# Kernel optimization log

Measured on AMD Instinct MI355X. Metric: run time of the kernel, lower is better.

## Reference

```python
import jax, jax.numpy as jnp
import numpy as np
from jax import lax

EPS = 1e-5


def _conv(x, w, b, stride, pad):
    # x: [B,C,H,W], w: [O,I,kh,kw] (NCHW / OIHW, same as torch Conv2d)
    y = lax.conv_general_dilated(
        x, w, window_strides=stride,
        padding=[(pad[0], pad[0]), (pad[1], pad[1])],
        dimension_numbers=('NCHW', 'OIHW', 'NCHW'))
    return y + b[None, :, None, None]


def _bn(x, gamma, beta, mean, var):
    # BatchNorm2d in eval mode (running statistics)
    inv = gamma / jnp.sqrt(var + EPS)
    return x * inv[None, :, None, None] + (beta - mean * inv)[None, :, None, None]


def _mask_time(x, lens):
    # Vectorized replacement of the per-sample narrow/fill loop:
    # zero every time step >= lens[b] along the last axis.
    t = jnp.arange(x.shape[3])
    keep = (t[None, :] < lens[:, None]).astype(x.dtype)  # [B, W]
    return x * keep[:, None, None, :]


def _new_len(lens, kernel_w, stride_w, pad_w):
    # matches get_new_sequence_lengths for Conv2d with dilation 1
    return (lens + 2 * pad_w - (kernel_w - 1) - 1) // stride_w + 1


def _forward(inputs, seq_lengths,
             w1, b1, g1, be1, m1, v1,
             w2, b2, g2, be2, m2, v2):
    lens = seq_lengths.astype(jnp.int32)
    # layer 1: Conv2d(1,32,(41,11),(2,2),(20,5))
    x = _conv(inputs, w1, b1, (2, 2), (20, 5))
    lens = _new_len(lens, 11, 2, 5)
    x = _mask_time(x, lens)
    # BatchNorm2d(32) -> mask
    x = _mask_time(_bn(x, g1, be1, m1, v1), lens)
    # Hardtanh(0,20) -> mask
    x = _mask_time(jnp.clip(x, 0.0, 20.0), lens)
    # layer 2: Conv2d(32,32,(21,11),(2,1),(10,5))
    x = _conv(x, w2, b2, (2, 1), (10, 5))
    lens = _new_len(lens, 11, 1, 5)
    x = _mask_time(x, lens)
    x = _mask_time(_bn(x, g2, be2, m2, v2), lens)
    x = _mask_time(jnp.clip(x, 0.0, 20.0), lens)
    return x, lens


def setup_inputs() -> dict:
    key = jax.random.key(0)
    ks = jax.random.split(key, 8)
    inputs = jax.random.normal(ks[0], (32, 1, 161, 1024), dtype=jnp.float32)
    seq_lengths = jax.random.randint(ks[1], (32,), 1, 1024, dtype=jnp.int32)
    w1 = jax.random.normal(ks[2], (32, 1, 41, 11), dtype=jnp.float32) * 0.05
    b1 = jax.random.normal(ks[3], (32,), dtype=jnp.float32) * 0.05
    w2 = jax.random.normal(ks[4], (32, 32, 21, 11), dtype=jnp.float32) * 0.02
    b2 = jax.random.normal(ks[5], (32,), dtype=jnp.float32) * 0.05
    g1 = jnp.ones((32,), jnp.float32)
    be1 = jnp.zeros((32,), jnp.float32)
    m1 = jax.random.normal(ks[6], (32,), dtype=jnp.float32) * 0.1
    v1 = jnp.ones((32,), jnp.float32)
    g2 = jnp.ones((32,), jnp.float32)
    be2 = jnp.zeros((32,), jnp.float32)
    m2 = jax.random.normal(ks[7], (32,), dtype=jnp.float32) * 0.1
    v2 = jnp.ones((32,), jnp.float32)
    return {"inputs": inputs, "seq_lengths": seq_lengths,
            "w1": w1, "b1": b1, "g1": g1, "be1": be1, "m1": m1, "v1": v1,
            "w2": w2, "b2": b2, "g2": g2, "be2": be2, "m2": m2, "v2": v2}


def reference(inputs, seq_lengths, w1, b1, g1, be1, m1, v1,
              w2, b2, g2, be2, m2, v2):
    return _forward(inputs, seq_lengths, w1, b1, g1, be1, m1, v1,
                    w2, b2, g2, be2, m2, v2)
```

## Files before the change

### kernel.cpp

```cpp
#include <hip/hip_runtime.h>
#include <math.h>

#define B_    32
#define H_IN  161
#define W_IN  1024
#define C1_   32
#define H1_   81
#define W1_   512
#define C2_   32
#define H2_   41
#define W2_   512

#define OUT_X_SZ ((size_t)B_ * C2_ * H2_ * W2_)

#define WF2_B    0u
#define WF1_B    473088u
#define SCSH_B   515072u
#define LENS1_B  515584u
#define XG_B     515712u

#define WF2_N    236544
#define WF1_N    20992

typedef __bf16 v8bf __attribute__((ext_vector_type(8)));
typedef float v16f __attribute__((ext_vector_type(16)));

static __device__ __forceinline__ unsigned short f2bf(float f) {
    unsigned int u = __float_as_uint(f);
    unsigned int r = (u + 0x7fffu + ((u >> 16) & 1u)) >> 16;
    return (unsigned short)r;
}

__global__ void prep_kernel(const float* __restrict__ w1, const float* __restrict__ b1,
                            const float* __restrict__ g1, const float* __restrict__ be1,
                            const float* __restrict__ m1, const float* __restrict__ v1,
                            const float* __restrict__ w2, const float* __restrict__ b2,
                            const float* __restrict__ g2, const float* __restrict__ be2,
                            const float* __restrict__ m2, const float* __restrict__ v2,
                            const int* __restrict__ lens,
                            unsigned short* __restrict__ wf1, unsigned short* __restrict__ wf2,
                            float* __restrict__ scsh, int* __restrict__ lens1,
                            float* __restrict__ out_lens)
{
    const int i = blockIdx.x * blockDim.x + threadIdx.x;
    const int stride = gridDim.x * blockDim.x;

    for (int idx = i; idx < WF2_N; idx += stride) {
        int j  = idx & 7;
        int l  = (idx >> 3) & 63;
        int f  = idx >> 9;
        int ch = f & 1;
        int kwkh = f >> 1;
        int kw = kwkh % 11;
        int kh = kwkh / 11;
        int oc = l & 31;
        int c  = ch * 16 + ((l >> 5) << 3) + j;
        wf2[idx] = f2bf(w2[((oc * 32 + c) * 21 + kh) * 11 + kw]);
    }
    for (int idx = i; idx < WF1_N; idx += stride) {
        int j  = idx & 7;
        int l  = (idx >> 3) & 63;
        int kh = idx >> 9;
        int k  = ((l >> 5) << 3) + j;
        int oc = l & 31;
        wf1[idx] = (k < 11) ? f2bf(w1[oc * 451 + kh * 11 + k]) : (unsigned short)0;
    }
    if (i < 32) {
        float s1 = g1[i] / sqrtf(v1[i] + 1e-5f);
        scsh[i]      = s1;
        scsh[32 + i] = b1[i] * s1 + be1[i] - m1[i] * s1;
        float s2 = g2[i] / sqrtf(v2[i] + 1e-5f);
        scsh[64 + i] = s2;
        scsh[96 + i] = b2[i] * s2 + be2[i] - m2[i] * s2;
        int l1 = (lens[i] - 1) / 2 + 1;
        if (l1 > W1_) l1 = W1_;
        lens1[i] = l1;
        out_lens[i] = (float)l1;
    }
}

__global__ __launch_bounds__(256) void conv1_mfma(
    const float* __restrict__ x,
    const unsigned short* __restrict__ wf1,
    const float* __restrict__ scsh,
    const int* __restrict__ lens1,
    unsigned short* __restrict__ xg)
{
    const int t    = threadIdx.x;
    const int lane = t & 63;
    const int l31  = lane & 31;
    const int lhi  = lane >> 5;
    const int wv   = t >> 6;
    const int w0   = blockIdx.x * 256;
    const int h    = blockIdx.y;
    const int b    = blockIdx.z;

    __shared__ unsigned int srow[2][264];

    v16f acc0, acc1;
#pragma unroll
    for (int i = 0; i < 16; ++i) { acc0[i] = 0.f; acc1[i] = 0.f; }

    const int r0 = 2 * h - 20;
    const int cb = 2 * w0 - 5;
    const float* xb = x + (size_t)b * (H_IN * W_IN);

    const int dwbase = wv * 64 + l31 + 4 * lhi;

    {
        float a0 = 0.f, a1 = 0.f, c0v = 0.f, c1v = 0.f;
        if (r0 >= 0 && r0 < H_IN) {
            const float* src = xb + (size_t)r0 * W_IN;
            int c0 = cb + 2 * t;
            if ((unsigned)c0 < (unsigned)W_IN)       a0 = src[c0];
            if ((unsigned)(c0 + 1) < (unsigned)W_IN) a1 = src[c0 + 1];
            if (t < 7) {
                int c1 = cb + 2 * (256 + t);
                if ((unsigned)c1 < (unsigned)W_IN)       c0v = src[c1];
                if ((unsigned)(c1 + 1) < (unsigned)W_IN) c1v = src[c1 + 1];
            }
        }
        srow[0][t] = (unsigned int)f2bf(a0) | ((unsigned int)f2bf(a1) << 16);
        if (t < 7)
            srow[0][256 + t] = (unsigned int)f2bf(c0v) | ((unsigned int)f2bf(c1v) << 16);
    }
    __syncthreads();

    for (int kh = 0; kh < 41; ++kh) {
        const int p = kh & 1;
        const int rn = r0 + kh + 1;
        const bool rv = (kh < 40) && (rn >= 0) && (rn < H_IN);

        float a0 = 0.f, a1 = 0.f, c0v = 0.f, c1v = 0.f;
        if (rv) {
            const float* src = xb + (size_t)rn * W_IN;
            int c0 = cb + 2 * t;
            if ((unsigned)c0 < (unsigned)W_IN)       a0 = src[c0];
            if ((unsigned)(c0 + 1) < (unsigned)W_IN) a1 = src[c0 + 1];
            if (t < 7) {
                int c1 = cb + 2 * (256 + t);
                if ((unsigned)c1 < (unsigned)W_IN)       c0v = src[c1];
                if ((unsigned)(c1 + 1) < (unsigned)W_IN) c1v = src[c1 + 1];
            }
        }

        const int r = r0 + kh;
        if (r >= 0 && r < H_IN) {
            uint4 a_u = *((const uint4*)wf1 + kh * 32 + lane);
            v8bf a = __builtin_bit_cast(v8bf, a_u);
            const unsigned int* bp = &srow[p][0];
            {
                int dw = dwbase;
                uint4 bu;
                bu.x = bp[dw]; bu.y = bp[dw + 1]; bu.z = bp[dw + 2]; bu.w = bp[dw + 3];
                v8bf bb = __builtin_bit_cast(v8bf, bu);
                acc0 = __builtin_amdgcn_mfma_f32_32x32x16_bf16(a, bb, acc0, 0, 0, 0);
            }
            {
                int dw = dwbase + 32;
                uint4 bu;
                bu.x = bp[dw]; bu.y = bp[dw + 1]; bu.z = bp[dw + 2]; bu.w = bp[dw + 3];
                v8bf bb = __builtin_bit_cast(v8bf, bu);
                acc1 = __builtin_amdgcn_mfma_f32_32x32x16_bf16(a, bb, acc1, 0, 0, 0);
            }
        }

        if (rv) {
            srow[p ^ 1][t] = (unsigned int)f2bf(a0) | ((unsigned int)f2bf(a1) << 16);
            if (t < 7)
                srow[p ^ 1][256 + t] = (unsigned int)f2bf(c0v) | ((unsigned int)f2bf(c1v) << 16);
        }
        __syncthreads();
    }

    const int l1 = lens1[b];
#pragma unroll
    for (int nt = 0; nt < 2; ++nt) {
        const int w = w0 + wv * 64 + nt * 32 + l31;
        const bool keep = (w < l1);
        unsigned short* dp = xg + (((size_t)b * H1_ + h) * W1_ + w) * 32;
#pragma unroll
        for (int rq = 0; rq < 4; ++rq) {
            unsigned int wd[2];
#pragma unroll
            for (int d = 0; d < 2; ++d) {
                int rg = rq * 4 + d * 2;
                int oc = 8 * rq + 4 * lhi + d * 2;
                float av0 = (nt == 0) ? acc0[rg]     : acc1[rg];
                float av1 = (nt == 0) ? acc0[rg + 1] : acc1[rg + 1];
                float v0 = fminf(fmaxf(fmaf(av0, scsh[oc],     scsh[32 + oc]), 0.f), 20.f);
                float v1 = fminf(fmaxf(fmaf(av1, scsh[oc + 1], scsh[33 + oc]), 0.f), 20.f);
                if (!keep) { v0 = 0.f; v1 = 0.f; }
                wd[d] = (unsigned int)f2bf(v0) | ((unsigned int)f2bf(v1) << 16);
            }
            uint2 u; u.x = wd[0]; u.y = wd[1];
            *(uint2*)(dp + 8 * rq + 4 * lhi) = u;
        }
    }
}

#define ROWB 21280

__global__ __launch_bounds__(256, 3) void conv2_mfma(
    const unsigned short* __restrict__ xg,
    const unsigned short* __restrict__ wf2,
    const float* __restrict__ scsh,
    const int* __restrict__ lens1,
    float* __restrict__ out)
{
    const int t    = threadIdx.x;
    const int lane = t & 63;
    const int l31  = lane & 31;
    const int lhi  = lane >> 5;
    const int wv   = t >> 6;
    const int w0B  = blockIdx.x * 256;
    const int h    = blockIdx.y;
    const int b    = blockIdx.z;

    __shared__ __align__(16) char sbuf[2 * ROWB];

    v16f acc0, acc1;
#pragma unroll
    for (int i = 0; i < 16; ++i) { acc0[i] = 0.f; acc1[i] = 0.f; }

    const int st_lds = (t >> 2) * 80 + (t & 3) * 16;
    const int rd_lds = (wv * 64 + l31) * 80 + lhi * 16;

    const unsigned short* xb = xg + (size_t)b * (H1_ * W1_ * 32);
    const int r0 = 2 * h - 10;

    {
        int r = r0;
        if (r >= 0 && r < H1_) {
            const unsigned short* xrow = xb + (size_t)r * (W1_ * 32);
#pragma unroll
            for (int it = 0; it < 5; ++it) {
                int i = t + it * 256;
                int wp = (i >> 2) + w0B - 5;
                uint4 z; z.x = z.y = z.z = z.w = 0u;
                if (i < 1064 && wp >= 0 && wp < W1_)
                    z = *(const uint4*)(xrow + (size_t)wp * 32 + (i & 3) * 8);
                if (i < 1064)
                    *(uint4*)(sbuf + st_lds + it * 5120) = z;
            }
        }
    }
    __syncthreads();

    for (int kh = 0; kh < 21; ++kh) {
        const int p = kh & 1;
        const int rn = r0 + kh + 1;
        const bool stage_next = (kh < 20) && (rn >= 0) && (rn < H1_);

        uint4 g0, g1, g2, g3, g4;
        g0.x=g0.y=g0.z=g0.w=0u; g1=g0; g2=g0; g3=g0; g4=g0;
        if (stage_next) {
            const unsigned short* xrow = xb + (size_t)rn * (W1_ * 32);
            const int wbase = (t >> 2) + w0B - 5;
            const int ck = (t & 3) * 8;
            if (wbase >= 0 && wbase < W1_)                 g0 = *(const uint4*)(xrow + (size_t)wbase * 32 + ck);
            if (wbase + 64 >= 0 && wbase + 64 < W1_)       g1 = *(const uint4*)(xrow + (size_t)(wbase + 64) * 32 + ck);
            if (wbase + 128 < W1_)                         g2 = *(const uint4*)(xrow + (size_t)(wbase + 128) * 32 + ck);
            if (wbase + 192 < W1_)                         g3 = *(const uint4*)(xrow + (size_t)(wbase + 192) * 32 + ck);
            if (t < 40 && wbase + 256 < W1_)               g4 = *(const uint4*)(xrow + (size_t)(wbase + 256) * 32 + ck);
        }

        const int r = r0 + kh;
        if (r >= 0 && r < H1_) {
            const unsigned short* wkh = wf2 + kh * (22 * 512);
            const char* bbase = sbuf + p * ROWB + rd_lds;
#pragma unroll
            for (int kw = 0; kw < 11; ++kw) {
#pragma unroll
                for (int ch = 0; ch < 2; ++ch) {
                    uint4 a_u = *((const uint4*)(wkh + ((kw * 2 + ch) << 9)) + lane);
                    uint4 b0_u = *(const uint4*)(bbase + kw * 80 + ch * 32);
                    uint4 b1_u = *(const uint4*)(bbase + 2560 + kw * 80 + ch * 32);
                    v8bf a  = __builtin_bit_cast(v8bf, a_u);
                    v8bf bb0 = __builtin_bit_cast(v8bf, b0_u);
                    v8bf bb1 = __builtin_bit_cast(v8bf, b1_u);
                    acc0 = __builtin_amdgcn_mfma_f32_32x32x16_bf16(a, bb0, acc0, 0, 0, 0);
                    acc1 = __builtin_amdgcn_mfma_f32_32x32x16_bf16(a, bb1, acc1, 0, 0, 0);
                }
            }
        }

        if (stage_next) {
            char* wb = sbuf + (p ^ 1) * ROWB + st_lds;
            *(uint4*)(wb)            = g0;
            *(uint4*)(wb + 5120)     = g1;
            *(uint4*)(wb + 2 * 5120) = g2;
            *(uint4*)(wb + 3 * 5120) = g3;
            if (t < 40) *(uint4*)(wb + 4 * 5120) = g4;
        }
        __syncthreads();
    }

    const int l2 = lens1[b];
#pragma unroll
    for (int nt = 0; nt < 2; ++nt) {
        const int w = w0B + wv * 64 + nt * 32 + l31;
        const bool keep = (w < l2);
#pragma unroll
        for (int reg = 0; reg < 16; ++reg) {
            int oc = (reg & 3) + 8 * (reg >> 2) + 4 * lhi;
            float av = (nt == 0) ? acc0[reg] : acc1[reg];
            float v = fmaf(av, scsh[64 + oc], scsh[96 + oc]);
            v = fminf(fmaxf(v, 0.f), 20.f);
            out[(((size_t)b * C2_ + oc) * H2_ + h) * W2_ + w] = keep ? v : 0.f;
        }
    }
}

extern "C" void kernel_launch(void* const* d_in, const int* in_sizes, int n_in,
                              void* d_out, int out_size, void* d_ws, size_t ws_size,
                              hipStream_t stream) {
    const float* inputs = (const float*)d_in[0];
    const int*   slen   = (const int*)d_in[1];
    const float* w1 = (const float*)d_in[2];
    const float* b1 = (const float*)d_in[3];
    const float* g1 = (const float*)d_in[4];
    const float* be1 = (const float*)d_in[5];
    const float* m1 = (const float*)d_in[6];
    const float* v1 = (const float*)d_in[7];
    const float* w2 = (const float*)d_in[8];
    const float* b2 = (const float*)d_in[9];
    const float* g2 = (const float*)d_in[10];
    const float* be2 = (const float*)d_in[11];
    const float* m2 = (const float*)d_in[12];
    const float* v2 = (const float*)d_in[13];

    char* ws = (char*)d_ws;
    unsigned short* wf2  = (unsigned short*)(ws + WF2_B);
    unsigned short* wf1  = (unsigned short*)(ws + WF1_B);
    float*          scsh = (float*)(ws + SCSH_B);
    int*            lens1 = (int*)(ws + LENS1_B);
    unsigned short* xg   = (unsigned short*)(ws + XG_B);

    float* out_x    = (float*)d_out;
    float* out_lens = out_x + OUT_X_SZ;

    hipLaunchKernelGGL(prep_kernel, dim3(256), dim3(256), 0, stream,
                       w1, b1, g1, be1, m1, v1, w2, b2, g2, be2, m2, v2,
                       slen, wf1, wf2, scsh, lens1, out_lens);

    hipLaunchKernelGGL(conv1_mfma, dim3(2, H1_, B_), dim3(256), 0, stream,
                       inputs, wf1, scsh, lens1, xg);

    hipLaunchKernelGGL(conv2_mfma, dim3(2, H2_, B_), dim3(256), 0, stream,
                       xg, wf2, scsh, lens1, out_x);
}
```

Before: 523.6 us.

## Compute four output rows per block and pre-convert input to padded bf16

Both convolutions now give each block four output rows, with a 128-wide column tile. Each staged input row feeds up to four accumulators, so the per-block row staging and barrier count drop sharply. The prep kernel now also writes a zero-padded bf16 copy of the input. Conv1 then reads its B operands straight from global memory instead of converting into LDS. The cost is an extra input conversion pass and more accumulator registers. Each weight fragment is also reused less, so more weight loads hit L2.

Result: slower. 748.7 us (+43.0%).

```diff
diff --git a/kernel.cpp b/kernel.cpp
--- a/kernel.cpp
+++ b/kernel.cpp
@@ -17,10 +17,13 @@
 #define WF1_B    473088u
 #define SCSH_B   515072u
 #define LENS1_B  515584u
-#define XG_B     515712u
+#define XBF_B    515712u
+#define XG_B     11314304u
 
 #define WF2_N    236544
 #define WF1_N    20992
+#define XBF_ROW  1048
+#define XBF_N    (32 * 161 * XBF_ROW)
 
 typedef __bf16 v8bf __attribute__((ext_vector_type(8)));
 typedef float v16f __attribute__((ext_vector_type(16)));
@@ -31,7 +34,8 @@
     return (unsigned short)r;
 }
 
-__global__ void prep_kernel(const float* __restrict__ w1, const float* __restrict__ b1,
+__global__ void prep_kernel(const float* __restrict__ x,
+                            const float* __restrict__ w1, const float* __restrict__ b1,
                             const float* __restrict__ g1, const float* __restrict__ be1,
                             const float* __restrict__ m1, const float* __restrict__ v1,
                             const float* __restrict__ w2, const float* __restrict__ b2,
@@ -39,12 +43,21 @@
                             const float* __restrict__ m2, const float* __restrict__ v2,
                             const int* __restrict__ lens,
                             unsigned short* __restrict__ wf1, unsigned short* __restrict__ wf2,
+                            unsigned short* __restrict__ xbf,
                             float* __restrict__ scsh, int* __restrict__ lens1,
                             float* __restrict__ out_lens)
 {
     const int i = blockIdx.x * blockDim.x + threadIdx.x;
     const int stride = gridDim.x * blockDim.x;
 
+    for (int idx = i; idx < XBF_N; idx += stride) {
+        int s  = idx % XBF_ROW;
+        int br = idx / XBF_ROW;
+        int c  = s - 5;
+        float v = 0.f;
+        if ((unsigned)c < (unsigned)W_IN) v = x[(size_t)br * W_IN + c];
+        xbf[idx] = f2bf(v);
+    }
     for (int idx = i; idx < WF2_N; idx += stride) {
         int j  = idx & 7;
         int l  = (idx >> 3) & 63;
@@ -80,7 +93,7 @@
 }
 
 __global__ __launch_bounds__(256) void conv1_mfma(
-    const float* __restrict__ x,
+    const unsigned short* __restrict__ xbf,
     const unsigned short* __restrict__ wf1,
     const float* __restrict__ scsh,
     const int* __restrict__ lens1,
@@ -91,115 +104,66 @@
     const int l31  = lane & 31;
     const int lhi  = lane >> 5;
     const int wv   = t >> 6;
-    const int w0   = blockIdx.x * 256;
-    const int h    = blockIdx.y;
+    const int W    = blockIdx.x * 128 + wv * 32;
+    const int h0   = blockIdx.y * 4;
     const int b    = blockIdx.z;
 
-    __shared__ unsigned int srow[2][264];
-
-    v16f acc0, acc1;
-#pragma unroll
-    for (int i = 0; i < 16; ++i) { acc0[i] = 0.f; acc1[i] = 0.f; }
-
-    const int r0 = 2 * h - 20;
-    const int cb = 2 * w0 - 5;
-    const float* xb = x + (size_t)b * (H_IN * W_IN);
-
-    const int dwbase = wv * 64 + l31 + 4 * lhi;
-
-    {
-        float a0 = 0.f, a1 = 0.f, c0v = 0.f, c1v = 0.f;
-        if (r0 >= 0 && r0 < H_IN) {
-            const float* src = xb + (size_t)r0 * W_IN;
-            int c0 = cb + 2 * t;
-            if ((unsigned)c0 < (unsigned)W_IN)       a0 = src[c0];
-            if ((unsigned)(c0 + 1) < (unsigned)W_IN) a1 = src[c0 + 1];
-            if (t < 7) {
-                int c1 = cb + 2 * (256 + t);
-                if ((unsigned)c1 < (unsigned)W_IN)       c0v = src[c1];
-                if ((unsigned)(c1 + 1) < (unsigned)W_IN) c1v = src[c1 + 1];
-            }
-        }
-        srow[0][t] = (unsigned int)f2bf(a0) | ((unsigned int)f2bf(a1) << 16);
-        if (t < 7)
-            srow[0][256 + t] = (unsigned int)f2bf(c0v) | ((unsigned int)f2bf(c1v) << 16);
-    }
-    __syncthreads();
-
-    for (int kh = 0; kh < 41; ++kh) {
-        const int p = kh & 1;
-        const int rn = r0 + kh + 1;
-        const bool rv = (kh < 40) && (rn >= 0) && (rn < H_IN);
-
-        float a0 = 0.f, a1 = 0.f, c0v = 0.f, c1v = 0.f;
-        if (rv) {
-            const float* src = xb + (size_t)rn * W_IN;
-            int c0 = cb + 2 * t;
-            if ((unsigned)c0 < (unsigned)W_IN)       a0 = src[c0];
-            if ((unsigned)(c0 + 1) < (unsigned)W_IN) a1 = src[c0 + 1];
-            if (t < 7) {
-                int c1 = cb + 2 * (256 + t);
-                if ((unsigned)c1 < (unsigned)W_IN)       c0v = src[c1];
-                if ((unsigned)(c1 + 1) < (unsigned)W_IN) c1v = src[c1 + 1];
-            }
-        }
-
-        const int r = r0 + kh;
-        if (r >= 0 && r < H_IN) {
-            uint4 a_u = *((const uint4*)wf1 + kh * 32 + lane);
-            v8bf a = __builtin_bit_cast(v8bf, a_u);
-            const unsigned int* bp = &srow[p][0];
-            {
-                int dw = dwbase;
-                uint4 bu;
-                bu.x = bp[dw]; bu.y = bp[dw + 1]; bu.z = bp[dw + 2]; bu.w = bp[dw + 3];
-                v8bf bb = __builtin_bit_cast(v8bf, bu);
-                acc0 = __builtin_amdgcn_mfma_f32_32x32x16_bf16(a, bb, acc0, 0, 0, 0);
-            }
-            {
-                int dw = dwbase + 32;
-                uint4 bu;
-                bu.x = bp[dw]; bu.y = bp[dw + 1]; bu.z = bp[dw + 2]; bu.w = bp[dw + 3];
-                v8bf bb = __builtin_bit_cast(v8bf, bu);
-                acc1 = __builtin_amdgcn_mfma_f32_32x32x16_bf16(a, bb, acc1, 0, 0, 0);
-            }
-        }
-
-        if (rv) {
-            srow[p ^ 1][t] = (unsigned int)f2bf(a0) | ((unsigned int)f2bf(a1) << 16);
-            if (t < 7)
-                srow[p ^ 1][256 + t] = (unsigned int)f2bf(c0v) | ((unsigned int)f2bf(c1v) << 16);
-        }
-        __syncthreads();
+    v16f acc[4];
+#pragma unroll
+    for (int hh = 0; hh < 4; ++hh)
+#pragma unroll
+        for (int i = 0; i < 16; ++i) acc[hh][i] = 0.f;
+
+    const char* xrow0 = (const char*)(xbf + (size_t)b * (H_IN * XBF_ROW));
+    const int boff = 4 * (W + l31) + 16 * lhi;
+
+    for (int rr = 0; rr < 47; ++rr) {
+        const int r = 2 * h0 - 20 + rr;
+        if (r < 0 || r >= H_IN) continue;
+
+        const unsigned int* bp = (const unsigned int*)(xrow0 + (size_t)r * (XBF_ROW * 2) + boff);
+        uint4 bu; bu.x = bp[0]; bu.y = bp[1]; bu.z = bp[2]; bu.w = bp[3];
+        v8bf bv = __builtin_bit_cast(v8bf, bu);
+
+#pragma unroll
+        for (int hh = 0; hh < 4; ++hh) {
+            const int kh = rr - 2 * hh;
+            if ((unsigned)kh < 41u && (h0 + hh) < H1_) {
+                uint4 au = *((const uint4*)wf1 + kh * 64 + lane);
+                acc[hh] = __builtin_amdgcn_mfma_f32_32x32x16_bf16(
+                    __builtin_bit_cast(v8bf, au), bv, acc[hh], 0, 0, 0);
+            }
+        }
     }
 
     const int l1 = lens1[b];
-#pragma unroll
-    for (int nt = 0; nt < 2; ++nt) {
-        const int w = w0 + wv * 64 + nt * 32 + l31;
-        const bool keep = (w < l1);
-        unsigned short* dp = xg + (((size_t)b * H1_ + h) * W1_ + w) * 32;
-#pragma unroll
-        for (int rq = 0; rq < 4; ++rq) {
-            unsigned int wd[2];
-#pragma unroll
-            for (int d = 0; d < 2; ++d) {
-                int rg = rq * 4 + d * 2;
-                int oc = 8 * rq + 4 * lhi + d * 2;
-                float av0 = (nt == 0) ? acc0[rg]     : acc1[rg];
-                float av1 = (nt == 0) ? acc0[rg + 1] : acc1[rg + 1];
-                float v0 = fminf(fmaxf(fmaf(av0, scsh[oc],     scsh[32 + oc]), 0.f), 20.f);
-                float v1 = fminf(fmaxf(fmaf(av1, scsh[oc + 1], scsh[33 + oc]), 0.f), 20.f);
-                if (!keep) { v0 = 0.f; v1 = 0.f; }
-                wd[d] = (unsigned int)f2bf(v0) | ((unsigned int)f2bf(v1) << 16);
-            }
-            uint2 u; u.x = wd[0]; u.y = wd[1];
-            *(uint2*)(dp + 8 * rq + 4 * lhi) = u;
-        }
-    }
-}
-
-#define ROWB 21280
+    const int w  = W + l31;
+    const bool keep = (w < l1);
+#pragma unroll
+    for (int hh = 0; hh < 4; ++hh) {
+        const int h = h0 + hh;
+        if (h < H1_) {
+            unsigned short* dp = xg + (((size_t)b * H1_ + h) * W1_ + w) * 32;
+#pragma unroll
+            for (int rq = 0; rq < 4; ++rq) {
+                unsigned int wd[2];
+#pragma unroll
+                for (int d = 0; d < 2; ++d) {
+                    int rg = rq * 4 + d * 2;
+                    int oc = 8 * rq + 4 * lhi + d * 2;
+                    float v0 = fminf(fmaxf(fmaf(acc[hh][rg],     scsh[oc],     scsh[32 + oc]), 0.f), 20.f);
+                    float v1 = fminf(fmaxf(fmaf(acc[hh][rg + 1], scsh[oc + 1], scsh[33 + oc]), 0.f), 20.f);
+                    if (!keep) { v0 = 0.f; v1 = 0.f; }
+                    wd[d] = (unsigned int)f2bf(v0) | ((unsigned int)f2bf(v1) << 16);
+                }
+                uint2 u; u.x = wd[0]; u.y = wd[1];
+                *(uint2*)(dp + 8 * rq + 4 * lhi) = u;
+            }
+        }
+    }
+}
+
+#define ROWB2 11040
 
 __global__ __launch_bounds__(256, 3) void conv2_mfma(
     const unsigned short* __restrict__ xg,
@@ -213,101 +177,109 @@
     const int l31  = lane & 31;
     const int lhi  = lane >> 5;
     const int wv   = t >> 6;
-    const int w0B  = blockIdx.x * 256;
-    const int h    = blockIdx.y;
+    const int w0   = blockIdx.x * 128;
+    const int h0   = blockIdx.y * 4;
     const int b    = blockIdx.z;
 
-    __shared__ __align__(16) char sbuf[2 * ROWB];
-
-    v16f acc0, acc1;
-#pragma unroll
-    for (int i = 0; i < 16; ++i) { acc0[i] = 0.f; acc1[i] = 0.f; }
-
-    const int st_lds = (t >> 2) * 80 + (t & 3) * 16;
-    const int rd_lds = (wv * 64 + l31) * 80 + lhi * 16;
+    __shared__ __align__(16) char sbuf[2 * ROWB2];
+
+    v16f acc[4];
+#pragma unroll
+    for (int hh = 0; hh < 4; ++hh)
+#pragma unroll
+        for (int i = 0; i < 16; ++i) acc[hh][i] = 0.f;
+
+    const int i1 = t + 256, i2 = t + 512;
+    const int st0 = (t >> 2) * 80 + (t & 3) * 16;
+    const int st1 = (i1 >> 2) * 80 + (i1 & 3) * 16;
+    const int st2 = (i2 >> 2) * 80 + (i2 & 3) * 16;
+    const int gw0 = w0 - 5 + (t >> 2);
+    const int gw1 = w0 - 5 + (i1 >> 2);
+    const int gw2 = w0 - 5 + (i2 >> 2);
+    const int gc0 = (t & 3) * 8, gc1 = (i1 & 3) * 8, gc2 = (i2 & 3) * 8;
 
     const unsigned short* xb = xg + (size_t)b * (H1_ * W1_ * 32);
-    const int r0 = 2 * h - 10;
-
-    {
-        int r = r0;
+    const int rbase = 2 * h0 - 10;
+
+    if (rbase >= 0 && rbase < H1_) {
+        const unsigned short* xr = xb + (size_t)rbase * (W1_ * 32);
+        uint4 z0 = {0,0,0,0}, z1 = {0,0,0,0}, z2 = {0,0,0,0};
+        if ((unsigned)gw0 < (unsigned)W1_) z0 = *(const uint4*)(xr + (size_t)gw0 * 32 + gc0);
+        if ((unsigned)gw1 < (unsigned)W1_) z1 = *(const uint4*)(xr + (size_t)gw1 * 32 + gc1);
+        if (t < 40 && (unsigned)gw2 < (unsigned)W1_) z2 = *(const uint4*)(xr + (size_t)gw2 * 32 + gc2);
+        *(uint4*)(sbuf + st0) = z0;
+        *(uint4*)(sbuf + st1) = z1;
+        if (t < 40) *(uint4*)(sbuf + st2) = z2;
+    }
+    __syncthreads();
+
+    const int bro = (wv * 32 + l31) * 80 + lhi * 16;
+
+    for (int rr = 0; rr < 27; ++rr) {
+        const int p  = rr & 1;
+        const int rn = rbase + rr + 1;
+        const bool sv = (rr < 26) && rn >= 0 && rn < H1_;
+
+        uint4 z0 = {0,0,0,0}, z1 = {0,0,0,0}, z2 = {0,0,0,0};
+        if (sv) {
+            const unsigned short* xr = xb + (size_t)rn * (W1_ * 32);
+            if ((unsigned)gw0 < (unsigned)W1_) z0 = *(const uint4*)(xr + (size_t)gw0 * 32 + gc0);
+            if ((unsigned)gw1 < (unsigned)W1_) z1 = *(const uint4*)(xr + (size_t)gw1 * 32 + gc1);
+            if (t < 40 && (unsigned)gw2 < (unsigned)W1_) z2 = *(const uint4*)(xr + (size_t)gw2 * 32 + gc2);
+        }
+
+        const int r = rbase + rr;
         if (r >= 0 && r < H1_) {
-            const unsigned short* xrow = xb + (size_t)r * (W1_ * 32);
-#pragma unroll
-            for (int it = 0; it < 5; ++it) {
-                int i = t + it * 256;
-                int wp = (i >> 2) + w0B - 5;
-                uint4 z; z.x = z.y = z.z = z.w = 0u;
-                if (i < 1064 && wp >= 0 && wp < W1_)
-                    z = *(const uint4*)(xrow + (size_t)wp * 32 + (i & 3) * 8);
-                if (i < 1064)
-                    *(uint4*)(sbuf + st_lds + it * 5120) = z;
-            }
-        }
-    }
-    __syncthreads();
-
-    for (int kh = 0; kh < 21; ++kh) {
-        const int p = kh & 1;
-        const int rn = r0 + kh + 1;
-        const bool stage_next = (kh < 20) && (rn >= 0) && (rn < H1_);
-
-        uint4 g0, g1, g2, g3, g4;
-        g0.x=g0.y=g0.z=g0.w=0u; g1=g0; g2=g0; g3=g0; g4=g0;
-        if (stage_next) {
-            const unsigned short* xrow = xb + (size_t)rn * (W1_ * 32);
-            const int wbase = (t >> 2) + w0B - 5;
-            const int ck = (t & 3) * 8;
-            if (wbase >= 0 && wbase < W1_)                 g0 = *(const uint4*)(xrow + (size_t)wbase * 32 + ck);
-            if (wbase + 64 >= 0 && wbase + 64 < W1_)       g1 = *(const uint4*)(xrow + (size_t)(wbase + 64) * 32 + ck);
-            if (wbase + 128 < W1_)                         g2 = *(const uint4*)(xrow + (size_t)(wbase + 128) * 32 + ck);
-            if (wbase + 192 < W1_)                         g3 = *(const uint4*)(xrow + (size_t)(wbase + 192) * 32 + ck);
-            if (t < 40 && wbase + 256 < W1_)               g4 = *(const uint4*)(xrow + (size_t)(wbase + 256) * 32 + ck);
-        }
-
-        const int r = r0 + kh;
-        if (r >= 0 && r < H1_) {
-            const unsigned short* wkh = wf2 + kh * (22 * 512);
-            const char* bbase = sbuf + p * ROWB + rd_lds;
-#pragma unroll
-            for (int kw = 0; kw < 11; ++kw) {
-#pragma unroll
-                for (int ch = 0; ch < 2; ++ch) {
-                    uint4 a_u = *((const uint4*)(wkh + ((kw * 2 + ch) << 9)) + lane);
-                    uint4 b0_u = *(const uint4*)(bbase + kw * 80 + ch * 32);
-                    uint4 b1_u = *(const uint4*)(bbase + 2560 + kw * 80 + ch * 32);
-                    v8bf a  = __builtin_bit_cast(v8bf, a_u);
-                    v8bf bb0 = __builtin_bit_cast(v8bf, b0_u);
-                    v8bf bb1 = __builtin_bit_cast(v8bf, b1_u);
-                    acc0 = __builtin_amdgcn_mfma_f32_32x32x16_bf16(a, bb0, acc0, 0, 0, 0);
-                    acc1 = __builtin_amdgcn_mfma_f32_32x32x16_bf16(a, bb1, acc1, 0, 0, 0);
+            const uint4* ap[4];
+            bool av[4];
+#pragma unroll
+            for (int hh = 0; hh < 4; ++hh) {
+                int kh = rr - 2 * hh;
+                av[hh] = ((unsigned)kh < 21u) && ((h0 + hh) < H2_);
+                ap[hh] = (const uint4*)wf2 + (size_t)(av[hh] ? kh : 0) * (22 * 64) + lane;
+            }
+            const char* bb = sbuf + p * ROWB2 + bro;
+#pragma unroll
+            for (int ch = 0; ch < 2; ++ch) {
+#pragma unroll
+                for (int kw = 0; kw < 11; ++kw) {
+                    uint4 bu = *(const uint4*)(bb + kw * 80 + ch * 32);
+                    v8bf bv = __builtin_bit_cast(v8bf, bu);
+#pragma unroll
+                    for (int hh = 0; hh < 4; ++hh) {
+                        if (av[hh]) {
+                            uint4 au = ap[hh][(kw * 2 + ch) * 64];
+                            acc[hh] = __builtin_amdgcn_mfma_f32_32x32x16_bf16(
+                                __builtin_bit_cast(v8bf, au), bv, acc[hh], 0, 0, 0);
+                        }
+                    }
                 }
             }
         }
 
-        if (stage_next) {
-            char* wb = sbuf + (p ^ 1) * ROWB + st_lds;
-            *(uint4*)(wb)            = g0;
-            *(uint4*)(wb + 5120)     = g1;
-            *(uint4*)(wb + 2 * 5120) = g2;
-            *(uint4*)(wb + 3 * 5120) = g3;
-            if (t < 40) *(uint4*)(wb + 4 * 5120) = g4;
+        if (sv) {
+            char* wb = sbuf + (p ^ 1) * ROWB2;
+            *(uint4*)(wb + st0) = z0;
+            *(uint4*)(wb + st1) = z1;
+            if (t < 40) *(uint4*)(wb + st2) = z2;
         }
         __syncthreads();
     }
 
     const int l2 = lens1[b];
-#pragma unroll
-    for (int nt = 0; nt < 2; ++nt) {
-        const int w = w0B + wv * 64 + nt * 32 + l31;
-        const bool keep = (w < l2);
-#pragma unroll
-        for (int reg = 0; reg < 16; ++reg) {
-            int oc = (reg & 3) + 8 * (reg >> 2) + 4 * lhi;
-            float av = (nt == 0) ? acc0[reg] : acc1[reg];
-            float v = fmaf(av, scsh[64 + oc], scsh[96 + oc]);
-            v = fminf(fmaxf(v, 0.f), 20.f);
-            out[(((size_t)b * C2_ + oc) * H2_ + h) * W2_ + w] = keep ? v : 0.f;
+    const int w  = w0 + wv * 32 + l31;
+    const bool keep = (w < l2);
+#pragma unroll
+    for (int hh = 0; hh < 4; ++hh) {
+        const int h = h0 + hh;
+        if (h < H2_) {
+#pragma unroll
+            for (int reg = 0; reg < 16; ++reg) {
+                int oc = (reg & 3) + 8 * (reg >> 2) + 4 * lhi;
+                float v = fmaf(acc[hh][reg], scsh[64 + oc], scsh[96 + oc]);
+                v = fminf(fmaxf(v, 0.f), 20.f);
+                out[(((size_t)b * C2_ + oc) * H2_ + h) * W2_ + w] = keep ? v : 0.f;
+            }
         }
     }
 }
@@ -335,18 +307,19 @@
     unsigned short* wf1  = (unsigned short*)(ws + WF1_B);
     float*          scsh = (float*)(ws + SCSH_B);
     int*            lens1 = (int*)(ws + LENS1_B);
+    unsigned short* xbf  = (unsigned short*)(ws + XBF_B);
     unsigned short* xg   = (unsigned short*)(ws + XG_B);
 
     float* out_x    = (float*)d_out;
     float* out_lens = out_x + OUT_X_SZ;
 
-    hipLaunchKernelGGL(prep_kernel, dim3(256), dim3(256), 0, stream,
-                       w1, b1, g1, be1, m1, v1, w2, b2, g2, be2, m2, v2,
-                       slen, wf1, wf2, scsh, lens1, out_lens);
-
-    hipLaunchKernelGGL(conv1_mfma, dim3(2, H1_, B_), dim3(256), 0, stream,
-                       inputs, wf1, scsh, lens1, xg);
-
-    hipLaunchKernelGGL(conv2_mfma, dim3(2, H2_, B_), dim3(256), 0, stream,
+    hipLaunchKernelGGL(prep_kernel, dim3(1024), dim3(256), 0, stream,
+                       inputs, w1, b1, g1, be1, m1, v1, w2, b2, g2, be2, m2, v2,
+                       slen, wf1, wf2, xbf, scsh, lens1, out_lens);
+
+    hipLaunchKernelGGL(conv1_mfma, dim3(4, 21, B_), dim3(256), 0, stream,
+                       xbf, wf1, scsh, lens1, xg);
+
+    hipLaunchKernelGGL(conv2_mfma, dim3(4, 11, B_), dim3(256), 0, stream,
                        xg, wf2, scsh, lens1, out_x);
 }
```
